# Optimization experiments

Hardware: AMD Instinct MI355X
Metric: run time of the kernel (lower is better)

## Reference

```python
import jax, jax.numpy as jnp
import numpy as np

BATCH = 16384
NNZ = 524288
INPUT_DIM = 30000
OUTPUT_DIM = 300


def setup_inputs() -> dict:
    key = jax.random.key(0)
    k1, k2, k3, k4 = jax.random.split(key, 4)
    sp_rows = jnp.sort(jax.random.randint(k1, (NNZ,), 0, BATCH, dtype=jnp.int32))
    sp_cols = jax.random.randint(k2, (NNZ,), 0, INPUT_DIM, dtype=jnp.int32)
    sp_vals = jax.random.uniform(k3, (NNZ,), dtype=jnp.float32)
    # glorot init for weights, zeros bias (as in the TF module)
    scale = jnp.sqrt(6.0 / (INPUT_DIM + OUTPUT_DIM)).astype(jnp.float32)
    weights = jax.random.uniform(k4, (INPUT_DIM, OUTPUT_DIM), dtype=jnp.float32,
                                 minval=-scale, maxval=scale)
    bias = jnp.zeros((OUTPUT_DIM,), dtype=jnp.float32)
    return {"sp_rows": sp_rows, "sp_cols": sp_cols, "sp_vals": sp_vals,
            "weights": weights, "bias": bias, "batch_size": BATCH}


def reference(sp_rows, sp_cols, sp_vals, weights, bias, batch_size):
    # sparse [batch, input_dim] @ dense [input_dim, output_dim]:
    # gather weight rows per nnz, scale by value, segment-sum into output rows.
    contrib = sp_vals[:, None] * weights[sp_cols]          # [nnz, output_dim]
    dense_vector = jax.ops.segment_sum(contrib, sp_rows,
                                       num_segments=batch_size)  # [batch, output_dim]
    dense_vector = dense_vector + bias
    return jax.nn.relu(dense_vector)
```

## Files before the change

### kernel.cpp

```cpp
#include <hip/hip_runtime.h>

#define OUT_DIM 300

typedef _Float16 half2_t __attribute__((ext_vector_type(2)));
typedef _Float16 half8_t __attribute__((ext_vector_type(8)));
typedef unsigned int uint32x4_t __attribute__((ext_vector_type(4)));

__global__ __launch_bounds__(256) void setup4_kernel(
    const int* __restrict__ rows, int* __restrict__ row_ptr,
    const float* __restrict__ w, unsigned char* __restrict__ wf,
    int nnz, int batch, int in_dim, int scat_blocks)
{
    if ((int)blockIdx.x < scat_blocks) {
        int i = blockIdx.x * 256 + threadIdx.x;
        if (i >= nnz) return;
        int r = rows[i];
        int prev = (i == 0) ? -1 : rows[i - 1];
        for (int q = prev + 1; q <= r; ++q) row_ptr[q] = i;
        if (i == nnz - 1)
            for (int q = r + 1; q <= batch; ++q) row_ptr[q] = nnz;
        return;
    }
    const int UPR = OUT_DIM / 2;
    int j = ((int)blockIdx.x - scat_blocks) * 256 + threadIdx.x;
    if (j >= in_dim * UPR) return;
    int r = j / UPR;
    int k = j - r * UPR;
    int s = k / 40; if (s > 3) s = 3;
    int kc = k - 40 * s;
    float2 f = *(const float2*)(w + (size_t)r * OUT_DIM + 2 * k);
    half2_t h;
    h.x = (_Float16)f.x;
    h.y = (_Float16)f.y;
    *(half2_t*)(wf + ((size_t)s * in_dim + r) * 160 + kc * 4) = h;
}

__global__ __launch_bounds__(256) void spmm4w(
    const int* __restrict__ row_ptr,
    const int* __restrict__ cols,
    const float* __restrict__ vals,
    const unsigned char* __restrict__ wf,
    const float* __restrict__ bias,
    float* __restrict__ out,
    int batch, int in_dim)
{
    __shared__ uint2 sh[4][76];

    const int slice = blockIdx.x & 3;
    const int wave  = threadIdx.x >> 6;
    const int lane  = threadIdx.x & 63;
    const int row   = (blockIdx.x >> 2) * 4 + wave;
    if (row >= batch) return;

    const int grp = lane / 10;
    const int ch  = lane - grp * 10;
    const int choff = ch * 16;

    const unsigned char* wslice = wf + (size_t)slice * in_dim * 160;

    __amdgpu_buffer_rsrc_t rsrc = __builtin_amdgcn_make_buffer_rsrc(
        (void*)wslice, (short)0, in_dim * 160, 0x00020000);

    uint2* shw = sh[wave];
    if (lane < 12) shw[64 + lane] = make_uint2(0u, 0u);

    const int lo = row_ptr[row];
    const int hi = row_ptr[row + 1];

    float a0 = 0.f, a1 = 0.f, a2 = 0.f, a3 = 0.f;
    float a4 = 0.f, a5 = 0.f, a6 = 0.f, a7 = 0.f;

    for (int base = lo; base < hi; base += 64) {
        const int rem = hi - base;
        const int cnt = rem < 64 ? rem : 64;

        uint2 ov = make_uint2(0u, 0u);
        if (lane < cnt) {
            ov.x = (unsigned)(cols[base + lane] * 160);
            ov.y = __float_as_uint(vals[base + lane]);
        }
        shw[lane] = ov;

        const int rr  = (cnt + 5) / 6;
        const int rrp = (rr + 3) & ~3;
        for (int r0 = 0; r0 < rrp; r0 += 4) {
#pragma unroll
            for (int u = 0; u < 4; ++u) {
                uint2 q = shw[6 * (r0 + u) + grp];
                float v = __uint_as_float(q.y);
                uint32x4_t raw = __builtin_amdgcn_raw_buffer_load_b128(
                    rsrc, (int)(q.x + choff), 0,  1);
                half8_t wv = __builtin_bit_cast(half8_t, raw);
                a0 += v * (float)wv[0];
                a1 += v * (float)wv[1];
                a2 += v * (float)wv[2];
                a3 += v * (float)wv[3];
                a4 += v * (float)wv[4];
                a5 += v * (float)wv[5];
                a6 += v * (float)wv[6];
                a7 += v * (float)wv[7];
            }
        }
    }

    a0 += __shfl_down(a0, 30); a1 += __shfl_down(a1, 30);
    a2 += __shfl_down(a2, 30); a3 += __shfl_down(a3, 30);
    a4 += __shfl_down(a4, 30); a5 += __shfl_down(a5, 30);
    a6 += __shfl_down(a6, 30); a7 += __shfl_down(a7, 30);

    float f0 = a0 + __shfl_down(a0, 10) + __shfl_down(a0, 20);
    float f1 = a1 + __shfl_down(a1, 10) + __shfl_down(a1, 20);
    float f2 = a2 + __shfl_down(a2, 10) + __shfl_down(a2, 20);
    float f3 = a3 + __shfl_down(a3, 10) + __shfl_down(a3, 20);
    float f4 = a4 + __shfl_down(a4, 10) + __shfl_down(a4, 20);
    float f5 = a5 + __shfl_down(a5, 10) + __shfl_down(a5, 20);
    float f6 = a6 + __shfl_down(a6, 10) + __shfl_down(a6, 20);
    float f7 = a7 + __shfl_down(a7, 10) + __shfl_down(a7, 20);

    const int nlan = (slice == 3) ? 8 : 10;
    if (lane < nlan) {
        const int col = slice * 80 + lane * 8;
        float* orow = out + (size_t)row * OUT_DIM + col;
        const float4 b0 = *(const float4*)(bias + col);
        float4 s0;
        s0.x = fmaxf(f0 + b0.x, 0.f);
        s0.y = fmaxf(f1 + b0.y, 0.f);
        s0.z = fmaxf(f2 + b0.z, 0.f);
        s0.w = fmaxf(f3 + b0.w, 0.f);
        *(float4*)orow = s0;
        if (slice < 3 || lane < 7) {
            const float4 b1 = *(const float4*)(bias + col + 4);
            float4 s1;
            s1.x = fmaxf(f4 + b1.x, 0.f);
            s1.y = fmaxf(f5 + b1.y, 0.f);
            s1.z = fmaxf(f6 + b1.z, 0.f);
            s1.w = fmaxf(f7 + b1.w, 0.f);
            *(float4*)(orow + 4) = s1;
        }
    }
}

__global__ __launch_bounds__(256) void row_ptr_scatter(
    const int* __restrict__ rows, int* __restrict__ row_ptr, int nnz, int batch)
{
    int i = blockIdx.x * 256 + threadIdx.x;
    if (i >= nnz) return;
    int r = rows[i];
    int prev = (i == 0) ? -1 : rows[i - 1];
    for (int q = prev + 1; q <= r; ++q) row_ptr[q] = i;
    if (i == nnz - 1)
        for (int q = r + 1; q <= batch; ++q) row_ptr[q] = nnz;
}

__global__ __launch_bounds__(256) void spmm_wave_f32_kernel(
    const int* __restrict__ row_ptr,
    const int* __restrict__ cols,
    const float* __restrict__ vals,
    const float* __restrict__ weights,
    const float* __restrict__ bias,
    float* __restrict__ out,
    int batch)
{
    const int wave = threadIdx.x >> 6;
    const int lane = threadIdx.x & 63;
    const int row  = blockIdx.x * 4 + wave;
    if (row >= batch) return;

    const int lo = row_ptr[row];
    const int hi = row_ptr[row + 1];
    float4 acc0 = make_float4(0.f, 0.f, 0.f, 0.f);
    float4 acc1 = make_float4(0.f, 0.f, 0.f, 0.f);
    const bool tail = (lane < 75 - 64);

    for (int base = lo; base < hi; base += 64) {
        const int rem = hi - base;
        const int cnt = rem < 64 ? rem : 64;
        int   c = 0;
        float v = 0.0f;
        if (lane < cnt) { c = cols[base + lane]; v = vals[base + lane]; }
        const int rounds = (cnt + 7) & ~7;
        for (int k = 0; k < rounds; k += 8) {
#pragma unroll
            for (int u = 0; u < 8; ++u) {
                const int   cc = __shfl(c, k + u);
                const float vv = __shfl(v, k + u);
                const float4* wrow = (const float4*)(weights + (size_t)cc * OUT_DIM);
                float4 w0 = wrow[lane];
                acc0.x += vv * w0.x; acc0.y += vv * w0.y;
                acc0.z += vv * w0.z; acc0.w += vv * w0.w;
                if (tail) {
                    float4 w1 = wrow[64 + lane];
                    acc1.x += vv * w1.x; acc1.y += vv * w1.y;
                    acc1.z += vv * w1.z; acc1.w += vv * w1.w;
                }
            }
        }
    }

    const float4* b4 = (const float4*)bias;
    float4* orow = (float4*)(out + (size_t)row * OUT_DIM);
    float4 b0 = b4[lane];
    float4 r0;
    r0.x = fmaxf(acc0.x + b0.x, 0.f);
    r0.y = fmaxf(acc0.y + b0.y, 0.f);
    r0.z = fmaxf(acc0.z + b0.z, 0.f);
    r0.w = fmaxf(acc0.w + b0.w, 0.f);
    orow[lane] = r0;
    if (tail) {
        float4 b1 = b4[64 + lane];
        float4 r1;
        r1.x = fmaxf(acc1.x + b1.x, 0.f);
        r1.y = fmaxf(acc1.y + b1.y, 0.f);
        r1.z = fmaxf(acc1.z + b1.z, 0.f);
        r1.w = fmaxf(acc1.w + b1.w, 0.f);
        orow[64 + lane] = r1;
    }
}

extern "C" void kernel_launch(void* const* d_in, const int* in_sizes, int n_in,
                              void* d_out, int out_size, void* d_ws, size_t ws_size,
                              hipStream_t stream) {
    const int*   sp_rows = (const int*)d_in[0];
    const int*   sp_cols = (const int*)d_in[1];
    const float* sp_vals = (const float*)d_in[2];
    const float* weights = (const float*)d_in[3];
    const float* bias    = (const float*)d_in[4];
    float* out = (float*)d_out;

    const int nnz    = in_sizes[0];
    const int w_elts = in_sizes[3];
    const int in_dim = w_elts / OUT_DIM;
    const int batch  = out_size / OUT_DIM;

    size_t rp_bytes = (size_t)(batch + 1) * sizeof(int);
    size_t wf_off   = (rp_bytes + 255) & ~(size_t)255;
    size_t need4    = wf_off + (size_t)in_dim * 4 * 160 + 256;

    int* row_ptr = (int*)d_ws;
    const int rowgroups = (batch + 3) / 4;

    if (ws_size >= need4) {
        unsigned char* wf = (unsigned char*)d_ws + wf_off;
        const int scat_blocks = (nnz + 255) / 256;
        const int rep_blocks  = (in_dim * (OUT_DIM / 2) + 255) / 256;
        setup4_kernel<<<scat_blocks + rep_blocks, 256, 0, stream>>>(
            sp_rows, row_ptr, weights, wf, nnz, batch, in_dim, scat_blocks);
        spmm4w<<<rowgroups * 4, 256, 0, stream>>>(
            row_ptr, sp_cols, sp_vals, wf, bias, out, batch, in_dim);
    } else {
        row_ptr_scatter<<<(nnz + 255) / 256, 256, 0, stream>>>(
            sp_rows, row_ptr, nnz, batch);
        spmm_wave_f32_kernel<<<(batch + 3) / 4, 256, 0, stream>>>(
            row_ptr, sp_cols, sp_vals, weights, bias, out, batch);
    }
}
```

Measured before the change: 136.9 us.

## Repack fp16 weights into five 128-byte column slices with XCD-aware block mapping

The fp16 weight copy is re-laid out as five slices of 64 columns (128 bytes per row) instead of four 160-byte slices. Each wave now uses 8 groups of 8 lanes, so the cross-lane reduction is a power-of-two shuffle tree and the shared-memory padding goes away. Blocks are remapped so that all row groups of one slice land on the same XCD, which should improve L2 reuse of that slice's weights. The cost is one more slice pass over the sparse indices per row, and the last slice is partly padding.

```diff
diff --git a/kernel.cpp b/kernel.cpp
--- a/kernel.cpp
+++ b/kernel.cpp
@@ -1,12 +1,13 @@
 #include <hip/hip_runtime.h>
 
 #define OUT_DIM 300
-
-typedef _Float16 half2_t __attribute__((ext_vector_type(2)));
+#define SLICES  5
+#define SLICE_B 128
+
 typedef _Float16 half8_t __attribute__((ext_vector_type(8)));
 typedef unsigned int uint32x4_t __attribute__((ext_vector_type(4)));
 
-__global__ __launch_bounds__(256) void setup4_kernel(
+__global__ __launch_bounds__(256) void setup5_kernel(
     const int* __restrict__ rows, int* __restrict__ row_ptr,
     const float* __restrict__ w, unsigned char* __restrict__ wf,
     int nnz, int batch, int in_dim, int scat_blocks)
@@ -21,49 +22,59 @@
             for (int q = r + 1; q <= batch; ++q) row_ptr[q] = nnz;
         return;
     }
-    const int UPR = OUT_DIM / 2;
     int j = ((int)blockIdx.x - scat_blocks) * 256 + threadIdx.x;
-    if (j >= in_dim * UPR) return;
-    int r = j / UPR;
-    int k = j - r * UPR;
-    int s = k / 40; if (s > 3) s = 3;
-    int kc = k - 40 * s;
-    float2 f = *(const float2*)(w + (size_t)r * OUT_DIM + 2 * k);
-    half2_t h;
-    h.x = (_Float16)f.x;
-    h.y = (_Float16)f.y;
-    *(half2_t*)(wf + ((size_t)s * in_dim + r) * 160 + kc * 4) = h;
-}
-
-__global__ __launch_bounds__(256) void spmm4w(
+    if (j >= in_dim * (SLICES * 8)) return;
+    int r   = j / 40;
+    int c16 = j - r * 40;
+    int s   = c16 >> 3;
+    int kc  = c16 & 7;
+    int c0  = c16 * 8;
+    const float* wr = w + (size_t)r * OUT_DIM + c0;
+    float4 f0 = make_float4(0.f, 0.f, 0.f, 0.f);
+    float4 f1 = make_float4(0.f, 0.f, 0.f, 0.f);
+    if (c0 + 4 <= OUT_DIM) f0 = *(const float4*)wr;
+    if (c0 + 8 <= OUT_DIM) f1 = *(const float4*)(wr + 4);
+    half8_t h;
+    h[0] = (_Float16)f0.x; h[1] = (_Float16)f0.y;
+    h[2] = (_Float16)f0.z; h[3] = (_Float16)f0.w;
+    h[4] = (_Float16)f1.x; h[5] = (_Float16)f1.y;
+    h[6] = (_Float16)f1.z; h[7] = (_Float16)f1.w;
+    *(half8_t*)(wf + ((size_t)s * in_dim + r) * SLICE_B + kc * 16) = h;
+}
+
+__global__ __launch_bounds__(256) void spmm5(
     const int* __restrict__ row_ptr,
     const int* __restrict__ cols,
     const float* __restrict__ vals,
     const unsigned char* __restrict__ wf,
     const float* __restrict__ bias,
     float* __restrict__ out,
-    int batch, int in_dim)
-{
-    __shared__ uint2 sh[4][76];
-
-    const int slice = blockIdx.x & 3;
-    const int wave  = threadIdx.x >> 6;
-    const int lane  = threadIdx.x & 63;
-    const int row   = (blockIdx.x >> 2) * 4 + wave;
+    int batch, int in_dim, int rowgroups)
+{
+    __shared__ uint2 sh[4][64];
+
+    const int nb  = (int)gridDim.x;
+    const int q8  = nb >> 3, rm = nb & 7;
+    const int xcd = (int)blockIdx.x & 7;
+    const int bi  = (int)blockIdx.x >> 3;
+    const int j   = (xcd < rm ? xcd * (q8 + 1)
+                              : rm * (q8 + 1) + (xcd - rm) * q8) + bi;
+    const int slice = j / rowgroups;
+    const int rg    = j - slice * rowgroups;
+
+    const int wave = threadIdx.x >> 6;
+    const int lane = threadIdx.x & 63;
+    const int row  = rg * 4 + wave;
     if (row >= batch) return;
 
-    const int grp = lane / 10;
-    const int ch  = lane - grp * 10;
-    const int choff = ch * 16;
-
-    const unsigned char* wslice = wf + (size_t)slice * in_dim * 160;
-
+    const int grp   = lane >> 3;
+    const int choff = (lane & 7) * 16;
+
+    const unsigned char* wslice = wf + (size_t)slice * in_dim * SLICE_B;
     __amdgpu_buffer_rsrc_t rsrc = __builtin_amdgcn_make_buffer_rsrc(
-        (void*)wslice, (short)0, in_dim * 160, 0x00020000);
+        (void*)wslice, (short)0, in_dim * SLICE_B, 0x00020000);
 
     uint2* shw = sh[wave];
-    if (lane < 12) shw[64 + lane] = make_uint2(0u, 0u);
-
     const int lo = row_ptr[row];
     const int hi = row_ptr[row + 1];
 
@@ -74,19 +85,22 @@
         const int rem = hi - base;
         const int cnt = rem < 64 ? rem : 64;
 
-        uint2 ov = make_uint2(0u, 0u);
+        uint2 ov;
         if (lane < cnt) {
-            ov.x = (unsigned)(cols[base + lane] * 160);
+            ov.x = (unsigned)cols[base + lane] * SLICE_B;
             ov.y = __float_as_uint(vals[base + lane]);
+        } else {
+            ov.x = 0x40000000u;
+            ov.y = 0u;
         }
         shw[lane] = ov;
 
-        const int rr  = (cnt + 5) / 6;
+        const int rr  = (cnt + 7) >> 3;
         const int rrp = (rr + 3) & ~3;
         for (int r0 = 0; r0 < rrp; r0 += 4) {
 #pragma unroll
             for (int u = 0; u < 4; ++u) {
-                uint2 q = shw[6 * (r0 + u) + grp];
+                uint2 q = shw[8 * (r0 + u) + grp];
                 float v = __uint_as_float(q.y);
                 uint32x4_t raw = __builtin_amdgcn_raw_buffer_load_b128(
                     rsrc, (int)(q.x + choff), 0,  1);
@@ -103,39 +117,39 @@
         }
     }
 
-    a0 += __shfl_down(a0, 30); a1 += __shfl_down(a1, 30);
-    a2 += __shfl_down(a2, 30); a3 += __shfl_down(a3, 30);
-    a4 += __shfl_down(a4, 30); a5 += __shfl_down(a5, 30);
-    a6 += __shfl_down(a6, 30); a7 += __shfl_down(a7, 30);
-
-    float f0 = a0 + __shfl_down(a0, 10) + __shfl_down(a0, 20);
-    float f1 = a1 + __shfl_down(a1, 10) + __shfl_down(a1, 20);
-    float f2 = a2 + __shfl_down(a2, 10) + __shfl_down(a2, 20);
-    float f3 = a3 + __shfl_down(a3, 10) + __shfl_down(a3, 20);
-    float f4 = a4 + __shfl_down(a4, 10) + __shfl_down(a4, 20);
-    float f5 = a5 + __shfl_down(a5, 10) + __shfl_down(a5, 20);
-    float f6 = a6 + __shfl_down(a6, 10) + __shfl_down(a6, 20);
-    float f7 = a7 + __shfl_down(a7, 10) + __shfl_down(a7, 20);
-
-    const int nlan = (slice == 3) ? 8 : 10;
-    if (lane < nlan) {
-        const int col = slice * 80 + lane * 8;
-        float* orow = out + (size_t)row * OUT_DIM + col;
-        const float4 b0 = *(const float4*)(bias + col);
-        float4 s0;
-        s0.x = fmaxf(f0 + b0.x, 0.f);
-        s0.y = fmaxf(f1 + b0.y, 0.f);
-        s0.z = fmaxf(f2 + b0.z, 0.f);
-        s0.w = fmaxf(f3 + b0.w, 0.f);
-        *(float4*)orow = s0;
-        if (slice < 3 || lane < 7) {
-            const float4 b1 = *(const float4*)(bias + col + 4);
-            float4 s1;
-            s1.x = fmaxf(f4 + b1.x, 0.f);
-            s1.y = fmaxf(f5 + b1.y, 0.f);
-            s1.z = fmaxf(f6 + b1.z, 0.f);
-            s1.w = fmaxf(f7 + b1.w, 0.f);
-            *(float4*)(orow + 4) = s1;
+    a0 += __shfl_down(a0, 32); a1 += __shfl_down(a1, 32);
+    a2 += __shfl_down(a2, 32); a3 += __shfl_down(a3, 32);
+    a4 += __shfl_down(a4, 32); a5 += __shfl_down(a5, 32);
+    a6 += __shfl_down(a6, 32); a7 += __shfl_down(a7, 32);
+    a0 += __shfl_down(a0, 16); a1 += __shfl_down(a1, 16);
+    a2 += __shfl_down(a2, 16); a3 += __shfl_down(a3, 16);
+    a4 += __shfl_down(a4, 16); a5 += __shfl_down(a5, 16);
+    a6 += __shfl_down(a6, 16); a7 += __shfl_down(a7, 16);
+    a0 += __shfl_down(a0, 8);  a1 += __shfl_down(a1, 8);
+    a2 += __shfl_down(a2, 8);  a3 += __shfl_down(a3, 8);
+    a4 += __shfl_down(a4, 8);  a5 += __shfl_down(a5, 8);
+    a6 += __shfl_down(a6, 8);  a7 += __shfl_down(a7, 8);
+
+    if (lane < 8) {
+        const int col = slice * 64 + lane * 8;
+        if (col + 4 <= OUT_DIM) {
+            float* orow = out + (size_t)row * OUT_DIM + col;
+            const float4 b0 = *(const float4*)(bias + col);
+            float4 s0;
+            s0.x = fmaxf(a0 + b0.x, 0.f);
+            s0.y = fmaxf(a1 + b0.y, 0.f);
+            s0.z = fmaxf(a2 + b0.z, 0.f);
+            s0.w = fmaxf(a3 + b0.w, 0.f);
+            *(float4*)orow = s0;
+            if (col + 8 <= OUT_DIM) {
+                const float4 b1 = *(const float4*)(bias + col + 4);
+                float4 s1;
+                s1.x = fmaxf(a4 + b1.x, 0.f);
+                s1.y = fmaxf(a5 + b1.y, 0.f);
+                s1.z = fmaxf(a6 + b1.z, 0.f);
+                s1.w = fmaxf(a7 + b1.w, 0.f);
+                *(float4*)(orow + 4) = s1;
+            }
         }
     }
 }
@@ -234,19 +248,19 @@
 
     size_t rp_bytes = (size_t)(batch + 1) * sizeof(int);
     size_t wf_off   = (rp_bytes + 255) & ~(size_t)255;
-    size_t need4    = wf_off + (size_t)in_dim * 4 * 160 + 256;
+    size_t need5    = wf_off + (size_t)in_dim * SLICES * SLICE_B + 256;
 
     int* row_ptr = (int*)d_ws;
     const int rowgroups = (batch + 3) / 4;
 
-    if (ws_size >= need4) {
+    if (ws_size >= need5) {
         unsigned char* wf = (unsigned char*)d_ws + wf_off;
         const int scat_blocks = (nnz + 255) / 256;
-        const int rep_blocks  = (in_dim * (OUT_DIM / 2) + 255) / 256;
-        setup4_kernel<<<scat_blocks + rep_blocks, 256, 0, stream>>>(
+        const int rep_blocks  = (in_dim * (SLICES * 8) + 255) / 256;
+        setup5_kernel<<<scat_blocks + rep_blocks, 256, 0, stream>>>(
             sp_rows, row_ptr, weights, wf, nnz, batch, in_dim, scat_blocks);
-        spmm4w<<<rowgroups * 4, 256, 0, stream>>>(
-            row_ptr, sp_cols, sp_vals, wf, bias, out, batch, in_dim);
+        spmm5<<<rowgroups * SLICES, 256, 0, stream>>>(
+            row_ptr, sp_cols, sp_vals, wf, bias, out, batch, in_dim, rowgroups);
     } else {
         row_ptr_scatter<<<(nnz + 255) / 256, 256, 0, stream>>>(
             sp_rows, row_ptr, nnz, batch);
```

After: 136.8 us. About the same (-0.1%).
